# Kernel tuning notes

Hardware: AMD Instinct MI355X
Metric: run time of the kernel (lower is better)

The kernel has to match this reference:

```python
import jax, jax.numpy as jnp
import numpy as np

B, S, D = 4, 2048, 1024
H = 16
HD = D // H  # 64

def setup_inputs() -> dict:
    key = jax.random.key(0)
    k1, k2, k3 = jax.random.split(key, 3)
    x = jax.random.normal(k1, (B, S, D), dtype=jnp.float32)
    w_qkv = jax.random.normal(k2, (D, 3 * D), dtype=jnp.float32) * 0.02
    w_proj = jax.random.normal(k3, (D, D), dtype=jnp.float32) * 0.02
    return {"x": x, "w_qkv": w_qkv, "w_proj": w_proj}

def reference(x, w_qkv, w_proj):
    b, s, d = x.shape
    qkv = x @ w_qkv                                  # [b,s,3d]
    q, k, v = jnp.split(qkv, 3, axis=2)
    # [b,s,d] -> [b,h,s,hd]
    q = q.reshape(b, s, H, HD).transpose(0, 2, 1, 3)
    k = k.reshape(b, s, H, HD).transpose(0, 2, 1, 3)
    v = v.reshape(b, s, H, HD).transpose(0, 2, 1, 3)
    att = jnp.einsum('bhqd,bhkd->bhqk', q, k) / jnp.sqrt(jnp.float32(HD))
    causal = jnp.tril(jnp.ones((s, s), dtype=bool))
    att = jnp.where(causal[None, None], att, jnp.float32(-jnp.inf))
    att = jax.nn.softmax(att, axis=-1)
    y = jnp.einsum('bhqk,bhkd->bhqd', att, v)        # [b,h,s,hd]
    y = y.transpose(0, 2, 1, 3).reshape(b, s, d)
    return y @ w_proj
```

## Files before the change

kernel.cpp:

```cpp
#include <hip/hip_runtime.h>
#include <stdint.h>

typedef unsigned short u16;
typedef __attribute__((ext_vector_type(8))) short bf16x8;
typedef __attribute__((ext_vector_type(4))) float f32x4;

__device__ __forceinline__ u16 f2bf(float f) {
  union { float f; unsigned u; } v; v.f = f;
  unsigned r = v.u + 0x7fffu + ((v.u >> 16) & 1u);
  return (u16)(r >> 16);
}

__device__ __forceinline__ void async_copy16(u16* lds_dst, const u16* g_src) {
  __builtin_amdgcn_global_load_lds(
      (const __attribute__((address_space(1))) unsigned*)(g_src),
      (__attribute__((address_space(3))) unsigned*)(lds_dst),
      16, 0, 0);
}

#define MFMA16(a, b, c) __builtin_amdgcn_mfma_f32_16x16x32_bf16((a), (b), (c), 0, 0, 0)

__global__ void cvt_bf16_kernel(const float* __restrict__ in, u16* __restrict__ out, int n4) {
  int i = blockIdx.x * blockDim.x + threadIdx.x;
  int stride = gridDim.x * blockDim.x;
  for (; i < n4; i += stride) {
    float4 v = ((const float4*)in)[i];
    ushort4 o;
    o.x = f2bf(v.x); o.y = f2bf(v.y); o.z = f2bf(v.z); o.w = f2bf(v.w);
    ((ushort4*)out)[i] = o;
  }
}

__global__ void transpose_cvt_kernel(const float* __restrict__ in, u16* __restrict__ out,
                                     int R, int C) {
  __shared__ float tile[32][33];
  int bx = blockIdx.x * 32;
  int by = blockIdx.y * 32;
  int tx = threadIdx.x & 31, ty = threadIdx.x >> 5;
#pragma unroll
  for (int j = 0; j < 32; j += 8)
    tile[ty + j][tx] = in[(size_t)(by + ty + j) * C + bx + tx];
  __syncthreads();
#pragma unroll
  for (int j = 0; j < 32; j += 8)
    out[(size_t)(bx + ty + j) * R + by + tx] = f2bf(tile[tx][ty + j]);
}

template<int MODE>
__global__ __launch_bounds__(256, 2)
void gemm2ph(const u16* __restrict__ A, const u16* __restrict__ BT,
             int K, int N,
             u16* __restrict__ q_o, u16* __restrict__ k_o, u16* __restrict__ vt_o,
             float* __restrict__ f_o) {
  __shared__ u16 As[2][128 * 64];
  __shared__ u16 Bs[2][128 * 64];

  const int t = threadIdx.x;
  const int w = t >> 6, l = t & 63;
  const int lr = l & 15, g = l >> 4;
  const int wm = (w >> 1) * 64, wn = (w & 1) * 64;
  const int m0 = blockIdx.x * 128, n0 = blockIdx.y * 128;

  const int r = t >> 3;
  const int sw = ((t & 7) * 16) ^ ((r & 7) << 4);
  const u16* pA = A + (size_t)(m0 + r) * K + (sw >> 1);
  const u16* pB = BT + (size_t)(n0 + r) * K + (sw >> 1);

#define STG(buf, kk)                                                    \
  do {                                                                  \
    async_copy16(&As[buf][t * 8],        pA + (kk));                    \
    async_copy16(&As[buf][2048 + t * 8], pA + (size_t)32 * K + (kk));   \
    async_copy16(&As[buf][4096 + t * 8], pA + (size_t)64 * K + (kk));   \
    async_copy16(&As[buf][6144 + t * 8], pA + (size_t)96 * K + (kk));   \
    async_copy16(&Bs[buf][t * 8],        pB + (kk));                    \
    async_copy16(&Bs[buf][2048 + t * 8], pB + (size_t)32 * K + (kk));   \
    async_copy16(&Bs[buf][4096 + t * 8], pB + (size_t)64 * K + (kk));   \
    async_copy16(&Bs[buf][6144 + t * 8], pB + (size_t)96 * K + (kk));   \
  } while (0)

  f32x4 acc[4][4] = {};

  STG(0, 0);
  __syncthreads();

  const int NTt = K / 64;
  for (int T = 0; T < NTt; ++T) {
    const int cur = T & 1;
    if (T + 1 < NTt) STG(cur ^ 1, (T + 1) * 64);

    bf16x8 af[4][2], bfr[4][2];
#pragma unroll
    for (int mf = 0; mf < 4; ++mf)
#pragma unroll
      for (int ks = 0; ks < 2; ++ks) {
        const int row = wm + mf * 16 + lr;
        af[mf][ks] = *(const bf16x8*)&As[cur][row * 64 + (((ks * 64 + g * 16) ^ ((row & 7) << 4)) >> 1)];
      }
#pragma unroll
    for (int nf = 0; nf < 4; ++nf)
#pragma unroll
      for (int ks = 0; ks < 2; ++ks) {
        const int row = wn + nf * 16 + lr;
        bfr[nf][ks] = *(const bf16x8*)&Bs[cur][row * 64 + (((ks * 64 + g * 16) ^ ((row & 7) << 4)) >> 1)];
      }
#pragma unroll
    for (int mf = 0; mf < 4; ++mf)
#pragma unroll
      for (int nf = 0; nf < 4; ++nf) {
        acc[mf][nf] = MFMA16(af[mf][0], bfr[nf][0], acc[mf][nf]);
        acc[mf][nf] = MFMA16(af[mf][1], bfr[nf][1], acc[mf][nf]);
      }
    __syncthreads();
  }
#undef STG

#pragma unroll
  for (int mf = 0; mf < 4; ++mf) {
#pragma unroll
    for (int nf = 0; nf < 4; ++nf) {
      const int col = n0 + wn + nf * 16 + lr;
#pragma unroll
      for (int j = 0; j < 4; ++j) {
        const int row = m0 + wm + mf * 16 + g * 4 + j;
        const float v = acc[mf][nf][j];
        if (MODE == 0) {
          const int which = col >> 10, rr = col & 1023;
          const int h = rr >> 6, hd = rr & 63;
          const int b = row >> 11, s = row & 2047;
          const size_t bh = (size_t)b * 16 + h;
          if (which == 0)      q_o[(bh * 2048 + s) * 64 + hd] = f2bf(v * 0.125f);
          else if (which == 1) k_o[(bh * 2048 + s) * 64 + hd] = f2bf(v);
          else                 vt_o[(bh * 64 + hd) * 2048 + s] = f2bf(v);
        } else {
          f_o[(size_t)row * N + col] = v;
        }
      }
    }
  }
}

__global__ __launch_bounds__(256, 2)
void attn_kernel(const u16* __restrict__ qws, const u16* __restrict__ kws,
                 const u16* __restrict__ vtws, u16* __restrict__ ybf) {
  __shared__ u16 Ksh[2][64 * 64];
  __shared__ u16 VTsh[2][64 * 64];
  __shared__ u16 Psh[4][32 * 64];

  const int bh = blockIdx.x & 63;
  const int qtile = 15 - (blockIdx.x >> 6);
  const int t = threadIdx.x;
  const int w = t >> 6, l = t & 63;
  const int lr = l & 15, g = l >> 4;
  const int q0 = qtile * 128 + w * 32;

  bf16x8 qf[2][2];
#pragma unroll
  for (int mf = 0; mf < 2; ++mf) {
    const u16* qb = qws + ((size_t)bh * 2048 + q0 + mf * 16 + lr) * 64 + g * 8;
#pragma unroll
    for (int ks = 0; ks < 2; ++ks) qf[mf][ks] = *(const bf16x8*)(qb + ks * 32);
  }

  f32x4 oacc[2][4] = {};
  float lrun[2][4] = {};

  const int srow = t >> 3;
  const int ssw = ((t & 7) * 16) ^ ((srow & 7) << 4);
  const u16* kb0 = kws + ((size_t)bh * 2048 + srow) * 64 + (ssw >> 1);
  const u16* vb0 = vtws + ((size_t)bh * 64 + srow) * 2048 + (ssw >> 1);

#define STAGE(kv0, buf)                                                \
  do {                                                                 \
    async_copy16(&Ksh[buf][t * 8],          kb0 + (size_t)(kv0)*64);   \
    async_copy16(&Ksh[buf][(t + 256) * 8],  kb0 + (size_t)((kv0)+32)*64); \
    async_copy16(&VTsh[buf][t * 8],         vb0 + (kv0));              \
    async_copy16(&VTsh[buf][(t + 256) * 8], vb0 + (size_t)32*2048 + (kv0)); \
  } while (0)

  const int nt = (qtile + 1) * 2;
  STAGE(0, 0);
  __syncthreads();

  for (int ti = 0; ti < nt; ++ti) {
    const int kv0 = ti * 64;
    const int cur = ti & 1;
    if (ti + 1 < nt) STAGE((ti + 1) * 64, cur ^ 1);

    if (kv0 <= q0 + 31) {
      const u16* Kc = Ksh[cur];
      const u16* Vc = VTsh[cur];

      f32x4 s[2][4] = {};
      __builtin_amdgcn_s_setprio(1);
#pragma unroll
      for (int f = 0; f < 4; ++f) {
        const int krow = f * 16 + lr;
        const int kswz = (krow & 7) << 4;
#pragma unroll
        for (int ks = 0; ks < 2; ++ks) {
          bf16x8 kb = *(const bf16x8*)&Kc[krow * 64 + (((ks * 64 + g * 16) ^ kswz) >> 1)];
          s[0][f] = MFMA16(qf[0][ks], kb, s[0][f]);
          s[1][f] = MFMA16(qf[1][ks], kb, s[1][f]);
        }
      }
      __builtin_amdgcn_s_setprio(0);

      const bool diag = (kv0 + 63 > q0);
#pragma unroll
      for (int mf = 0; mf < 2; ++mf)
#pragma unroll
        for (int f = 0; f < 4; ++f)
#pragma unroll
          for (int j = 0; j < 4; ++j) {
            float p = __expf(s[mf][f][j]);
            if (diag) {
              const int key = kv0 + f * 16 + lr;
              const int qrow = q0 + mf * 16 + g * 4 + j;
              p = (key <= qrow) ? p : 0.f;
            }
            s[mf][f][j] = p;
            lrun[mf][j] += p;
          }

#pragma unroll
      for (int mf = 0; mf < 2; ++mf)
#pragma unroll
        for (int f = 0; f < 4; ++f)
#pragma unroll
          for (int j = 0; j < 4; ++j) {
            const int prow = mf * 16 + g * 4 + j;
            Psh[w][prow * 64 + (((f * 32 + lr * 2) ^ ((prow & 7) << 4)) >> 1)] =
                f2bf(s[mf][f][j]);
          }

#pragma unroll
      for (int ks = 0; ks < 2; ++ks) {
        bf16x8 pa[2];
#pragma unroll
        for (int mf = 0; mf < 2; ++mf) {
          const int prow = mf * 16 + lr;
          pa[mf] = *(const bf16x8*)&Psh[w][prow * 64 + (((ks * 64 + g * 16) ^ ((prow & 7) << 4)) >> 1)];
        }
        __builtin_amdgcn_s_setprio(1);
#pragma unroll
        for (int nf = 0; nf < 4; ++nf) {
          const int vrow = nf * 16 + lr;
          bf16x8 vb = *(const bf16x8*)&Vc[vrow * 64 + (((ks * 64 + g * 16) ^ ((vrow & 7) << 4)) >> 1)];
          oacc[0][nf] = MFMA16(pa[0], vb, oacc[0][nf]);
          oacc[1][nf] = MFMA16(pa[1], vb, oacc[1][nf]);
        }
        __builtin_amdgcn_s_setprio(0);
      }
    }
    __syncthreads();
  }
#undef STAGE

  float linv[2][4];
#pragma unroll
  for (int mf = 0; mf < 2; ++mf)
#pragma unroll
    for (int j = 0; j < 4; ++j) {
      float s = lrun[mf][j];
#pragma unroll
      for (int d = 1; d < 16; d <<= 1) s += __shfl_xor(s, d, 64);
      linv[mf][j] = 1.f / s;
    }

  const int b = bh >> 4, h = bh & 15;
#pragma unroll
  for (int mf = 0; mf < 2; ++mf)
#pragma unroll
    for (int nf = 0; nf < 4; ++nf) {
      const int col = nf * 16 + lr;
#pragma unroll
      for (int j = 0; j < 4; ++j) {
        const int row = q0 + mf * 16 + g * 4 + j;
        const float o = oacc[mf][nf][j] * linv[mf][j];
        ybf[((size_t)b * 2048 + row) * 1024 + h * 64 + col] = f2bf(o);
      }
    }
}

extern "C" void kernel_launch(void* const* d_in, const int* in_sizes, int n_in,
                              void* d_out, int out_size, void* d_ws, size_t ws_size,
                              hipStream_t stream) {
  const float* x     = (const float*)d_in[0];
  const float* wqkv  = (const float*)d_in[1];
  const float* wproj = (const float*)d_in[2];
  float* out = (float*)d_out;

  char* ws = (char*)d_ws;
  u16* xbf    = (u16*)ws;
  u16* ybf    = xbf;
  u16* wqkvT  = (u16*)(ws + 16777216);
  u16* wprojT = (u16*)(ws + 16777216 + 6291456);
  u16* qws    = (u16*)(ws + 25165824);
  u16* kws    = (u16*)(ws + 41943040);
  u16* vtws   = (u16*)(ws + 58720256);

  cvt_bf16_kernel<<<2048, 256, 0, stream>>>(x, xbf, (8192 * 1024) / 4);
  transpose_cvt_kernel<<<dim3(3072 / 32, 1024 / 32), 256, 0, stream>>>(wqkv, wqkvT, 1024, 3072);
  transpose_cvt_kernel<<<dim3(1024 / 32, 1024 / 32), 256, 0, stream>>>(wproj, wprojT, 1024, 1024);
  gemm2ph<0><<<dim3(64, 24), 256, 0, stream>>>(xbf, wqkvT, 1024, 3072, qws, kws, vtws, nullptr);
  attn_kernel<<<16 * 64, 256, 0, stream>>>(qws, kws, vtws, ybf);
  gemm2ph<1><<<dim3(64, 8), 256, 0, stream>>>(ybf, wprojT, 1024, 1024, nullptr, nullptr, nullptr, out);
}
```

Measured before the change: 183.1 us.

## Replace QKV GEMM with 256x256-tile 8-wave kernel using 8-phase interleaved pipeline

Adds a new QKV projection GEMM that uses 512-thread blocks and 256x256 output tiles, with each wave computing a 128x64 sub-tile. The main loop is split into eight phases that interleave LDS reads, async global-to-LDS copies and MFMA bursts, separated by explicit barriers, waitcnt instructions and setprio. The aim is more operand reuse per tile and better overlap of memory traffic with matrix math in the largest GEMM. The cost is a hand-tuned schedule with many barriers, higher register pressure from 32 accumulator tiles, and a fixed K=1024 assumption. The output projection GEMM loses its template mode but is otherwise unchanged.

```diff
diff --git a/kernel.cpp b/kernel.cpp
--- a/kernel.cpp
+++ b/kernel.cpp
@@ -19,6 +19,8 @@
 }
 
 #define MFMA16(a, b, c) __builtin_amdgcn_mfma_f32_16x16x32_bf16((a), (b), (c), 0, 0, 0)
+#define BARRIER() asm volatile("s_barrier" ::: "memory")
+#define WAIT_LGKM0() do { asm volatile("s_waitcnt lgkmcnt(0)" ::: "memory"); __builtin_amdgcn_sched_barrier(0); } while (0)
 
 __global__ void cvt_bf16_kernel(const float* __restrict__ in, u16* __restrict__ out, int n4) {
   int i = blockIdx.x * blockDim.x + threadIdx.x;
@@ -46,12 +48,163 @@
     out[(size_t)(bx + ty + j) * R + by + tx] = f2bf(tile[tx][ty + j]);
 }
 
-template<int MODE>
+__global__ __launch_bounds__(512, 2)
+void gemm8ph(const u16* __restrict__ A, const u16* __restrict__ BT,
+             u16* __restrict__ q_o, u16* __restrict__ k_o, u16* __restrict__ vt_o) {
+  constexpr int K = 1024;
+  constexpr int NTI = 8;
+  __shared__ u16 As[2][2][8192];
+  __shared__ u16 Bs[2][2][8192];
+
+  const int t = threadIdx.x;
+  const int w = t >> 6, l = t & 63;
+  const int lr = l & 15, g = l >> 4;
+  const int wm = w >> 2, wn = w & 3;
+  const int m0 = blockIdx.x * 256, n0 = blockIdx.y * 256;
+
+  const int r = t >> 3;
+  const int sw = ((t & 7) * 16) ^ ((r & 7) << 4);
+  const u16* pA = A + (size_t)(m0 + r) * K + (sw >> 1);
+  const u16* pB = BT + (size_t)(n0 + r) * K + (sw >> 1);
+
+#define STGA(par, h, kk)                                                          \
+  do {                                                                            \
+    async_copy16(&As[par][h][t * 8],        pA + (size_t)((h) * 128) * K + (kk)); \
+    async_copy16(&As[par][h][4096 + t * 8], pA + (size_t)((h) * 128 + 64) * K + (kk)); \
+  } while (0)
+#define STGB(par, h, kk)                                                          \
+  do {                                                                            \
+    async_copy16(&Bs[par][h][t * 8],        pB + (size_t)((h) * 128) * K + (kk)); \
+    async_copy16(&Bs[par][h][4096 + t * 8], pB + (size_t)((h) * 128 + 64) * K + (kk)); \
+  } while (0)
+
+  f32x4 acc[8][4] = {};
+
+  STGB(0, 0, 0); STGB(0, 1, 0); STGA(0, 0, 0); STGA(0, 1, 0);
+  STGB(1, 0, 64); STGB(1, 1, 64); STGA(1, 0, 64);
+  asm volatile("s_waitcnt vmcnt(6)" ::: "memory");
+  BARRIER();
+
+  const int bh_ = wn >> 1;
+  const int br0 = (wn & 1) * 64;
+
+  bf16x8 a03[4][2], a47[4][2], bb[4][2];
+
+#define RD_A(par, dst, rbase)                                                       \
+  _Pragma("unroll") for (int mf = 0; mf < 4; ++mf)                                  \
+  _Pragma("unroll") for (int ks = 0; ks < 2; ++ks) {                                \
+    const int r2 = (rbase) + mf * 16 + lr;                                          \
+    dst[mf][ks] = *(const bf16x8*)&As[par][wm][r2 * 64 + (((ks * 64 + g * 16) ^ ((r2 & 7) << 4)) >> 1)]; \
+  }
+#define RD_B(par, nf0, nf1)                                                         \
+  _Pragma("unroll") for (int nf = (nf0); nf < (nf1); ++nf)                          \
+  _Pragma("unroll") for (int ks = 0; ks < 2; ++ks) {                                \
+    const int r2 = br0 + nf * 16 + lr;                                              \
+    bb[nf][ks] = *(const bf16x8*)&Bs[par][bh_][r2 * 64 + (((ks * 64 + g * 16) ^ ((r2 & 7) << 4)) >> 1)]; \
+  }
+#define MFMA_Q(mbase, nf0, nf1, asrc)                                               \
+  __builtin_amdgcn_s_setprio(1);                                                    \
+  _Pragma("unroll") for (int mf = 0; mf < 4; ++mf)                                  \
+  _Pragma("unroll") for (int nf = (nf0); nf < (nf1); ++nf) {                        \
+    acc[(mbase) + mf][nf] = MFMA16(asrc[mf][0], bb[nf][0], acc[(mbase) + mf][nf]);  \
+    acc[(mbase) + mf][nf] = MFMA16(asrc[mf][1], bb[nf][1], acc[(mbase) + mf][nf]);  \
+  }                                                                                 \
+  __builtin_amdgcn_s_setprio(0);                                                    \
+  __builtin_amdgcn_sched_barrier(0)
+
+  for (int it = 0; it < NTI; ++it) {
+    const int k1 = (2 * it + 1) * 64, k2 = (2 * it + 2) * 64, k3 = (2 * it + 3) * 64;
+    const bool st2 = (2 * it + 2) < (K / 64), st3 = (2 * it + 3) < (K / 64);
+
+    RD_A(0, a03, 0)
+    RD_B(0, 0, 2)
+    STGA(1, 1, k1);
+    asm volatile("s_waitcnt lgkmcnt(8)" ::: "memory");
+    BARRIER();
+    WAIT_LGKM0();
+    MFMA_Q(0, 0, 2, a03);
+    BARRIER();
+
+    RD_B(0, 2, 4)
+    if (st2) STGB(0, 0, k2);
+    BARRIER();
+    WAIT_LGKM0();
+    MFMA_Q(0, 2, 4, a03);
+    BARRIER();
+
+    RD_A(0, a47, 64)
+    if (st2) STGB(0, 1, k2);
+    BARRIER();
+    WAIT_LGKM0();
+    MFMA_Q(4, 0, 2, a47);
+    BARRIER();
+
+    if (st2) STGA(0, 0, k2);
+    if (it < NTI - 1) asm volatile("s_waitcnt vmcnt(6)" ::: "memory");
+    else              asm volatile("s_waitcnt vmcnt(0)" ::: "memory");
+    BARRIER();
+    MFMA_Q(4, 2, 4, a47);
+    BARRIER();
+
+    RD_A(1, a03, 0)
+    RD_B(1, 0, 2)
+    if (st2) STGA(0, 1, k2);
+    asm volatile("s_waitcnt lgkmcnt(8)" ::: "memory");
+    BARRIER();
+    WAIT_LGKM0();
+    MFMA_Q(0, 0, 2, a03);
+    BARRIER();
+
+    RD_B(1, 2, 4)
+    if (st3) STGB(1, 0, k3);
+    BARRIER();
+    WAIT_LGKM0();
+    MFMA_Q(0, 2, 4, a03);
+    BARRIER();
+
+    RD_A(1, a47, 64)
+    if (st3) STGB(1, 1, k3);
+    BARRIER();
+    WAIT_LGKM0();
+    MFMA_Q(4, 0, 2, a47);
+    BARRIER();
+
+    if (st3) STGA(1, 0, k3);
+    if (it < NTI - 1) asm volatile("s_waitcnt vmcnt(6)" ::: "memory");
+    BARRIER();
+    MFMA_Q(4, 2, 4, a47);
+    BARRIER();
+  }
+#undef RD_A
+#undef RD_B
+#undef MFMA_Q
+#undef STGA
+#undef STGB
+
+#pragma unroll
+  for (int mf = 0; mf < 8; ++mf) {
+#pragma unroll
+    for (int nf = 0; nf < 4; ++nf) {
+      const int col = n0 + wn * 64 + nf * 16 + lr;
+#pragma unroll
+      for (int j = 0; j < 4; ++j) {
+        const int row = m0 + wm * 128 + mf * 16 + g * 4 + j;
+        const float v = acc[mf][nf][j];
+        const int which = col >> 10, rr = col & 1023;
+        const int h = rr >> 6, hd = rr & 63;
+        const int b = row >> 11, s = row & 2047;
+        const size_t bh = (size_t)b * 16 + h;
+        if (which == 0)      q_o[(bh * 2048 + s) * 64 + hd] = f2bf(v * 0.125f);
+        else if (which == 1) k_o[(bh * 2048 + s) * 64 + hd] = f2bf(v);
+        else                 vt_o[(bh * 64 + hd) * 2048 + s] = f2bf(v);
+      }
+    }
+  }
+}
+
 __global__ __launch_bounds__(256, 2)
 void gemm2ph(const u16* __restrict__ A, const u16* __restrict__ BT,
-             int K, int N,
-             u16* __restrict__ q_o, u16* __restrict__ k_o, u16* __restrict__ vt_o,
-             float* __restrict__ f_o) {
+             int K, int N, float* __restrict__ f_o) {
   __shared__ u16 As[2][128 * 64];
   __shared__ u16 Bs[2][128 * 64];
 
@@ -115,28 +268,16 @@
 #undef STG
 
 #pragma unroll
-  for (int mf = 0; mf < 4; ++mf) {
+  for (int mf = 0; mf < 4; ++mf)
 #pragma unroll
     for (int nf = 0; nf < 4; ++nf) {
       const int col = n0 + wn + nf * 16 + lr;
 #pragma unroll
       for (int j = 0; j < 4; ++j) {
         const int row = m0 + wm + mf * 16 + g * 4 + j;
-        const float v = acc[mf][nf][j];
-        if (MODE == 0) {
-          const int which = col >> 10, rr = col & 1023;
-          const int h = rr >> 6, hd = rr & 63;
-          const int b = row >> 11, s = row & 2047;
-          const size_t bh = (size_t)b * 16 + h;
-          if (which == 0)      q_o[(bh * 2048 + s) * 64 + hd] = f2bf(v * 0.125f);
-          else if (which == 1) k_o[(bh * 2048 + s) * 64 + hd] = f2bf(v);
-          else                 vt_o[(bh * 64 + hd) * 2048 + s] = f2bf(v);
-        } else {
-          f_o[(size_t)row * N + col] = v;
-        }
+        f_o[(size_t)row * N + col] = acc[mf][nf][j];
       }
     }
-  }
 }
 
 __global__ __launch_bounds__(256, 2)
@@ -302,7 +443,7 @@
   cvt_bf16_kernel<<<2048, 256, 0, stream>>>(x, xbf, (8192 * 1024) / 4);
   transpose_cvt_kernel<<<dim3(3072 / 32, 1024 / 32), 256, 0, stream>>>(wqkv, wqkvT, 1024, 3072);
   transpose_cvt_kernel<<<dim3(1024 / 32, 1024 / 32), 256, 0, stream>>>(wproj, wprojT, 1024, 1024);
-  gemm2ph<0><<<dim3(64, 24), 256, 0, stream>>>(xbf, wqkvT, 1024, 3072, qws, kws, vtws, nullptr);
+  gemm8ph<<<dim3(32, 12), 512, 0, stream>>>(xbf, wqkvT, qws, kws, vtws);
   attn_kernel<<<16 * 64, 256, 0, stream>>>(qws, kws, vtws, ybf);
-  gemm2ph<1><<<dim3(64, 8), 256, 0, stream>>>(ybf, wprojT, 1024, 1024, nullptr, nullptr, nullptr, out);
-}
+  gemm2ph<<<dim3(64, 8), 256, 0, stream>>>(ybf, wprojT, 1024, 1024, out);
+}
```

After: 196.3 us. 7.2% more time.

## Use 32x32 MFMA with transposed scores to keep P in registers

Applied to the files above, without the earlier changes.

Rewrites the attention inner loop around 32x32x16 bf16 MFMA, computing K·Qᵀ so each lane holds one query row's scores. P is packed to bf16 with v_cvt_pk_bf16_f32 and lanes exchange halves with v_permlane32_swap, so it feeds the PV MFMA straight from registers. This removes the per-wave LDS staging buffer and its write/read round trip. The row-sum reduction shrinks to a single shuffle, and output stores become packed 8-byte writes. It depends on gfx950-specific instructions and on the lane layout mapping being exactly right.

```diff
diff --git a/kernel.cpp b/kernel.cpp
--- a/kernel.cpp
+++ b/kernel.cpp
@@ -2,14 +2,23 @@
 #include <stdint.h>
 
 typedef unsigned short u16;
+typedef unsigned int u32;
 typedef __attribute__((ext_vector_type(8))) short bf16x8;
 typedef __attribute__((ext_vector_type(4))) float f32x4;
+typedef __attribute__((ext_vector_type(16))) float f32x16;
 
 __device__ __forceinline__ u16 f2bf(float f) {
   union { float f; unsigned u; } v; v.f = f;
   unsigned r = v.u + 0x7fffu + ((v.u >> 16) & 1u);
   return (u16)(r >> 16);
 }
+
+__device__ __forceinline__ u32 pk_bf16(float lo, float hi) {
+  u32 r;
+  asm("v_cvt_pk_bf16_f32 %0, %1, %2" : "=v"(r) : "v"(lo), "v"(hi));
+  return r;
+}
+#define PLSWAP(a, b) asm volatile("v_permlane32_swap_b32 %0, %1" : "+v"(a), "+v"(b))
 
 __device__ __forceinline__ void async_copy16(u16* lds_dst, const u16* g_src) {
   __builtin_amdgcn_global_load_lds(
@@ -19,6 +28,7 @@
 }
 
 #define MFMA16(a, b, c) __builtin_amdgcn_mfma_f32_16x16x32_bf16((a), (b), (c), 0, 0, 0)
+#define MFMA32(a, b, c) __builtin_amdgcn_mfma_f32_32x32x16_bf16((a), (b), (c), 0, 0, 0)
 
 __global__ void cvt_bf16_kernel(const float* __restrict__ in, u16* __restrict__ out, int n4) {
   int i = blockIdx.x * blockDim.x + threadIdx.x;
@@ -144,25 +154,25 @@
                  const u16* __restrict__ vtws, u16* __restrict__ ybf) {
   __shared__ u16 Ksh[2][64 * 64];
   __shared__ u16 VTsh[2][64 * 64];
-  __shared__ u16 Psh[4][32 * 64];
 
   const int bh = blockIdx.x & 63;
   const int qtile = 15 - (blockIdx.x >> 6);
   const int t = threadIdx.x;
   const int w = t >> 6, l = t & 63;
-  const int lr = l & 15, g = l >> 4;
+  const int lq = l & 31;
+  const int h = l >> 5;
   const int q0 = qtile * 128 + w * 32;
-
-  bf16x8 qf[2][2];
-#pragma unroll
-  for (int mf = 0; mf < 2; ++mf) {
-    const u16* qb = qws + ((size_t)bh * 2048 + q0 + mf * 16 + lr) * 64 + g * 8;
-#pragma unroll
-    for (int ks = 0; ks < 2; ++ks) qf[mf][ks] = *(const bf16x8*)(qb + ks * 32);
-  }
-
-  f32x4 oacc[2][4] = {};
-  float lrun[2][4] = {};
+  const int qg = q0 + lq;
+
+  bf16x8 qf[4];
+  {
+    const u16* qb = qws + ((size_t)bh * 2048 + qg) * 64 + h * 8;
+#pragma unroll
+    for (int s = 0; s < 4; ++s) qf[s] = *(const bf16x8*)(qb + s * 16);
+  }
+
+  f32x16 oacc[2] = {};
+  float lsum = 0.f;
 
   const int srow = t >> 3;
   const int ssw = ((t & 7) * 16) ^ ((srow & 7) << 4);
@@ -190,95 +200,82 @@
       const u16* Kc = Ksh[cur];
       const u16* Vc = VTsh[cur];
 
-      f32x4 s[2][4] = {};
+      f32x16 st[2] = {};
       __builtin_amdgcn_s_setprio(1);
 #pragma unroll
-      for (int f = 0; f < 4; ++f) {
-        const int krow = f * 16 + lr;
-        const int kswz = (krow & 7) << 4;
-#pragma unroll
-        for (int ks = 0; ks < 2; ++ks) {
-          bf16x8 kb = *(const bf16x8*)&Kc[krow * 64 + (((ks * 64 + g * 16) ^ kswz) >> 1)];
-          s[0][f] = MFMA16(qf[0][ks], kb, s[0][f]);
-          s[1][f] = MFMA16(qf[1][ks], kb, s[1][f]);
+      for (int kt = 0; kt < 2; ++kt) {
+        const int row = kt * 32 + lq;
+        const int swz = (row & 7) << 4;
+#pragma unroll
+        for (int s = 0; s < 4; ++s) {
+          bf16x8 kf = *(const bf16x8*)&Kc[row * 64 + (((s * 32 + h * 16) ^ swz) >> 1)];
+          st[kt] = MFMA32(kf, qf[s], st[kt]);
         }
       }
       __builtin_amdgcn_s_setprio(0);
 
       const bool diag = (kv0 + 63 > q0);
 #pragma unroll
-      for (int mf = 0; mf < 2; ++mf)
-#pragma unroll
-        for (int f = 0; f < 4; ++f)
-#pragma unroll
-          for (int j = 0; j < 4; ++j) {
-            float p = __expf(s[mf][f][j]);
-            if (diag) {
-              const int key = kv0 + f * 16 + lr;
-              const int qrow = q0 + mf * 16 + g * 4 + j;
-              p = (key <= qrow) ? p : 0.f;
-            }
-            s[mf][f][j] = p;
-            lrun[mf][j] += p;
+      for (int kt = 0; kt < 2; ++kt)
+#pragma unroll
+        for (int p = 0; p < 16; ++p) {
+          float e = __expf(st[kt][p]);
+          if (diag) {
+            const int key = kv0 + kt * 32 + (p & 3) + 8 * (p >> 2) + 4 * h;
+            e = (key <= qg) ? e : 0.f;
           }
-
-#pragma unroll
-      for (int mf = 0; mf < 2; ++mf)
-#pragma unroll
-        for (int f = 0; f < 4; ++f)
-#pragma unroll
-          for (int j = 0; j < 4; ++j) {
-            const int prow = mf * 16 + g * 4 + j;
-            Psh[w][prow * 64 + (((f * 32 + lr * 2) ^ ((prow & 7) << 4)) >> 1)] =
-                f2bf(s[mf][f][j]);
-          }
-
-#pragma unroll
-      for (int ks = 0; ks < 2; ++ks) {
-        bf16x8 pa[2];
-#pragma unroll
-        for (int mf = 0; mf < 2; ++mf) {
-          const int prow = mf * 16 + lr;
-          pa[mf] = *(const bf16x8*)&Psh[w][prow * 64 + (((ks * 64 + g * 16) ^ ((prow & 7) << 4)) >> 1)];
-        }
-        __builtin_amdgcn_s_setprio(1);
-#pragma unroll
-        for (int nf = 0; nf < 4; ++nf) {
-          const int vrow = nf * 16 + lr;
-          bf16x8 vb = *(const bf16x8*)&Vc[vrow * 64 + (((ks * 64 + g * 16) ^ ((vrow & 7) << 4)) >> 1)];
-          oacc[0][nf] = MFMA16(pa[0], vb, oacc[0][nf]);
-          oacc[1][nf] = MFMA16(pa[1], vb, oacc[1][nf]);
-        }
-        __builtin_amdgcn_s_setprio(0);
-      }
+          st[kt][p] = e;
+          lsum += e;
+        }
+
+      bf16x8 pb[4];
+#pragma unroll
+      for (int kt = 0; kt < 2; ++kt)
+#pragma unroll
+        for (int s2l = 0; s2l < 2; ++s2l) {
+          const int p0 = s2l * 8;
+          u32 L0 = pk_bf16(st[kt][p0 + 0], st[kt][p0 + 1]);
+          u32 L1 = pk_bf16(st[kt][p0 + 2], st[kt][p0 + 3]);
+          u32 H0 = pk_bf16(st[kt][p0 + 4], st[kt][p0 + 5]);
+          u32 H1 = pk_bf16(st[kt][p0 + 6], st[kt][p0 + 7]);
+          PLSWAP(L0, H0);
+          PLSWAP(L1, H1);
+          union { u32 u[4]; bf16x8 v; } pw;
+          pw.u[0] = L0; pw.u[1] = L1; pw.u[2] = H0; pw.u[3] = H1;
+          pb[kt * 2 + s2l] = pw.v;
+        }
+
+      __builtin_amdgcn_s_setprio(1);
+#pragma unroll
+      for (int dt = 0; dt < 2; ++dt) {
+        const int row = dt * 32 + lq;
+        const int swz = (row & 7) << 4;
+#pragma unroll
+        for (int s2 = 0; s2 < 4; ++s2) {
+          bf16x8 vf = *(const bf16x8*)&Vc[row * 64 + (((s2 * 32 + h * 16) ^ swz) >> 1)];
+          oacc[dt] = MFMA32(vf, pb[s2], oacc[dt]);
+        }
+      }
+      __builtin_amdgcn_s_setprio(0);
     }
     __syncthreads();
   }
 #undef STAGE
 
-  float linv[2][4];
-#pragma unroll
-  for (int mf = 0; mf < 2; ++mf)
-#pragma unroll
-    for (int j = 0; j < 4; ++j) {
-      float s = lrun[mf][j];
-#pragma unroll
-      for (int d = 1; d < 16; d <<= 1) s += __shfl_xor(s, d, 64);
-      linv[mf][j] = 1.f / s;
-    }
-
-  const int b = bh >> 4, h = bh & 15;
-#pragma unroll
-  for (int mf = 0; mf < 2; ++mf)
-#pragma unroll
-    for (int nf = 0; nf < 4; ++nf) {
-      const int col = nf * 16 + lr;
-#pragma unroll
-      for (int j = 0; j < 4; ++j) {
-        const int row = q0 + mf * 16 + g * 4 + j;
-        const float o = oacc[mf][nf][j] * linv[mf][j];
-        ybf[((size_t)b * 2048 + row) * 1024 + h * 64 + col] = f2bf(o);
-      }
+  lsum += __shfl_xor(lsum, 32, 64);
+  const float linv = 1.f / lsum;
+
+  const int b = bh >> 4, hh = bh & 15;
+  u16* yb = ybf + ((size_t)b * 2048 + qg) * 1024 + hh * 64;
+#pragma unroll
+  for (int dt = 0; dt < 2; ++dt)
+#pragma unroll
+    for (int pg = 0; pg < 4; ++pg) {
+      u32 w0 = pk_bf16(oacc[dt][pg * 4 + 0] * linv, oacc[dt][pg * 4 + 1] * linv);
+      u32 w1 = pk_bf16(oacc[dt][pg * 4 + 2] * linv, oacc[dt][pg * 4 + 3] * linv);
+      union { u32 u[2]; unsigned long long ll; } pk2;
+      pk2.u[0] = w0; pk2.u[1] = w1;
+      *(unsigned long long*)(yb + dt * 32 + 8 * pg + 4 * h) = pk2.ll;
     }
 }
 
```

New measurement: 176.4 us. 3.6% less time.
